# Performance work log

Hardware: AMD Instinct MI355X
Metric: run time of the kernel (lower is better)

## Reference

```python
import jax, jax.numpy as jnp
import numpy as np

B = 131072      # batch
UNITS = 32      # state dim (Dense output)
HID = 1024      # hard-coded hidden width in HopfieldLayer
DT = 0.1
T = 1.0
N_STEPS = int(round(T / DT))  # 10 RK4 steps


def setup_inputs() -> dict:
    key = jax.random.key(0)
    k0, k1, k2 = jax.random.split(key, 3)
    x = jax.random.normal(k0, (B, UNITS), dtype=jnp.float32)
    # glorot-uniform style init as in keras Dense defaults (scale only matters for realism)
    lim1 = float(np.sqrt(6.0 / (UNITS + HID)))
    lim2 = float(np.sqrt(6.0 / (HID + UNITS)))
    W1 = jax.random.uniform(k1, (UNITS, HID), jnp.float32, -lim1, lim1)
    W2 = jax.random.uniform(k2, (HID, UNITS), jnp.float32, -lim2, lim2)
    b1 = jnp.zeros((HID,), jnp.float32)
    b2 = jnp.zeros((UNITS,), jnp.float32)
    return {"x": x, "W1": W1, "b1": b1, "W2": W2, "b2": b2}


def reference(x, W1, b1, W2, b2):
    dt = jnp.float32(DT)

    def energy_sum(z):
        # E(z) = 8 * || Dense2(relu(Dense1(z))) ||_2  (per sample), summed over batch
        h = jax.nn.relu(z @ W1 + b1)          # [B, HID]
        y = h @ W2 + b2                        # [B, UNITS]
        return jnp.sum(8.0 * jnp.sqrt(jnp.sum(y * y, axis=1)))

    def pvf(z):
        # Hopfield phase vector field: dx/dt = -grad_x E(x); linear_transform = identity
        return -jax.grad(energy_sum)(z)

    def rk4_step(z, _):
        k1 = pvf(z)
        k2 = pvf(z + 0.5 * dt * k1)
        k3 = pvf(z + 0.5 * dt * k2)
        k4 = pvf(z + dt * k3)
        z_next = z + (dt / 6.0) * (k1 + 2.0 * k2 + 2.0 * k3 + k4)
        return z_next, None

    y, _ = jax.lax.scan(rk4_step, x, None, length=N_STEPS)
    return y
```

## Files before the change

### kernel.cpp

```cpp
#include <hip/hip_runtime.h>

typedef _Float16 f16;
typedef __attribute__((ext_vector_type(8))) _Float16 f16x8;
typedef __attribute__((ext_vector_type(16))) float f32x16;
typedef __attribute__((ext_vector_type(2))) unsigned int u32x2;
typedef __attribute__((ext_vector_type(4))) unsigned int u32x4;
typedef unsigned int u32;
typedef unsigned short u16;

#define UNITS 32
#define HID   1024
#define NCH   32
#define TPB   256
#define WPB   4
#define SPB   128
#define NBLK  1024
#define BWDOFF 262144

static_assert(NBLK * SPB == 131072, "grid covers batch");

__global__ void prep_weights(const float* __restrict__ W1,
                             const float* __restrict__ W2,
                             f16* __restrict__ ws) {
    int idx = blockIdx.x * 256 + threadIdx.x;
    int c = idx >> 10, rem = idx & 1023;
    int jl = rem >> 5, u = rem & 31;
    int j = c * 32 + jl;
    float w1 = W1[u * HID + j];
    f16 h1 = (f16)w1;
    f16 l1 = (f16)(w1 - (float)h1);
    float w2 = W2[j * UNITS + u];
    f16 h2 = (f16)w2;
    f16 l2 = (f16)(w2 - (float)h2);
    char* p = (char*)ws;
    auto off = [&](int region, int slice, int row, int k) {
        int ks = k >> 4;
        int lane = row + ((k >> 3) & 1) * 32;
        return region + c * 8192 + (slice * 2 + ks) * 1024 + lane * 16 + (k & 7) * 2;
    };
    *(f16*)(p + off(0, 0, jl, u))      = h1;
    *(f16*)(p + off(0, 1, jl, u))      = l1;
    *(f16*)(p + off(0, 2, u, jl))      = h2;
    *(f16*)(p + off(0, 3, u, jl))      = l2;
    *(f16*)(p + off(BWDOFF, 0, jl, u)) = h2;
    *(f16*)(p + off(BWDOFF, 1, jl, u)) = l2;
    *(f16*)(p + off(BWDOFF, 2, u, jl)) = h1;
    *(f16*)(p + off(BWDOFF, 3, u, jl)) = l1;
}

__device__ __forceinline__ void plswap(u32& a, u32& b) {
    u32x2 r = __builtin_amdgcn_permlane32_swap(a, b, false, false);
    a = r.x; b = r.y;
}

__device__ __forceinline__ float fmix_lo(u32 h, float v, float fone) {
    float r;
    asm("v_fma_mix_f32 %0, -%1, %2, %3 op_sel_hi:[1,0,0]"
        : "=v"(r) : "v"(h), "v"(fone), "v"(v));
    return r;
}
__device__ __forceinline__ float fmix_hi(u32 h, float v, float fone) {
    float r;
    asm("v_fma_mix_f32 %0, -%1, %2, %3 op_sel:[1,0,0] op_sel_hi:[1,0,0]"
        : "=v"(r) : "v"(h), "v"(fone), "v"(v));
    return r;
}

#define LOADSET4(S, base) {                                               \
    const char* p_ = (base);                                              \
    S##0 = *(const f16x8*)(p_);                                           \
    S##1 = *(const f16x8*)(p_ + 1024);                                    \
    S##2 = *(const f16x8*)(p_ + 2048);                                    \
    S##3 = *(const f16x8*)(p_ + 3072); }

#define BUILD_FRAGS(F0, F1, L0, L1, V) {                                  \
    u32 owh[8], owl[8];                                                   \
    _Pragma("unroll")                                                     \
    for (int i_ = 0; i_ < 8; ++i_) {                                      \
        float v0_ = (V)[2*i_], v1_ = (V)[2*i_ + 1];                       \
        auto hp_ = __builtin_amdgcn_cvt_pkrtz(v0_, v1_);                  \
        owh[i_] = __builtin_bit_cast(u32, hp_);                           \
        float r0_ = fmix_lo(owh[i_], v0_, fone);                          \
        float r1_ = fmix_hi(owh[i_], v1_, fone);                          \
        auto lp_ = __builtin_amdgcn_cvt_pkrtz(r0_, r1_);                  \
        owl[i_] = __builtin_bit_cast(u32, lp_);                           \
    }                                                                     \
    {                                                                     \
        u32 a0_ = owh[0], b0_ = owh[2]; plswap(a0_, b0_);                 \
        u32 a1_ = owh[1], b1_ = owh[3]; plswap(a1_, b1_);                 \
        F0 = __builtin_bit_cast(f16x8, (u32x4){a0_, a1_, b0_, b1_});      \
        u32 c0_ = owh[4], d0_ = owh[6]; plswap(c0_, d0_);                 \
        u32 c1_ = owh[5], d1_ = owh[7]; plswap(c1_, d1_);                 \
        F1 = __builtin_bit_cast(f16x8, (u32x4){c0_, c1_, d0_, d1_});      \
        u32 e0_ = owl[0], f0_ = owl[2]; plswap(e0_, f0_);                 \
        u32 e1_ = owl[1], f1_ = owl[3]; plswap(e1_, f1_);                 \
        L0 = __builtin_bit_cast(f16x8, (u32x4){e0_, e1_, f0_, f1_});      \
        u32 g0_ = owl[4], h0_ = owl[6]; plswap(g0_, h0_);                 \
        u32 g1_ = owl[5], h1_ = owl[7]; plswap(g1_, h1_);                 \
        L1 = __builtin_bit_cast(f16x8, (u32x4){g0_, g1_, h0_, h1_});      \
    } }

#define MFMA(d, a, b, c) d = __builtin_amdgcn_mfma_f32_32x32x16_f16(a, b, c, 0, 0, 0)

__global__ __launch_bounds__(TPB, 2)
__attribute__((amdgpu_waves_per_eu(2, 2)))
void hopfield_mfma4(const float* __restrict__ x,
                    const float* __restrict__ b1,
                    const float* __restrict__ b2,
                    const f16* __restrict__ ws,
                    float* __restrict__ out) {
    __shared__ __align__(16) float sB1p[HID];
    __shared__ __align__(16) float sB2p[UNITS];
    __shared__ u16 sMsk[WPB][NCH * 64];

    const int tid = threadIdx.x;
    const int wv = tid >> 6, ln = tid & 63;
    const int s32 = ln & 31, gh = ln >> 5;

    for (int i = tid; i < HID; i += TPB) {
        int c = i >> 5, g_ = (i >> 4) & 1, r = i & 15;
        sB1p[i] = b1[c * 32 + ((r & 3) + ((r >> 2) << 3) + (g_ << 2))];
    }
    if (tid < UNITS) {
        int g_ = (tid >> 4) & 1, r = tid & 15;
        sB2p[tid] = b2[(r & 3) + ((r >> 2) << 3) + (g_ << 2)];
    }
    __syncthreads();

    u16* mkb = &sMsk[wv][0];
    const float fone = 1.0f;

    const long samp = (long)blockIdx.x * SPB + wv * 32 + s32;
    float zb[16], acc[16];
    {
        const float* xr = x + samp * UNITS;
        #pragma unroll
        for (int q = 0; q < 4; ++q) {
            float4 v = *(const float4*)(xr + 8 * q + 4 * gh);
            zb[4*q+0] = v.x; zb[4*q+1] = v.y; zb[4*q+2] = v.z; zb[4*q+3] = v.w;
        }
    }

    f32x16 zeros;
    #pragma unroll
    for (int r = 0; r < 16; ++r) zeros[r] = 0.f;

    const char* pfwd = (const char*)ws + (size_t)ln * 16;
    const char* pbwd = pfwd + BWDOFF;

    f16x8 P0, P1, P2, P3;
    f16x8 Q0, Q1, Q2, Q3;
    LOADSET4(P, pfwd)

    f16x8 za0h, za1h, za0l, za1l;
    BUILD_FRAGS(za0h, za1h, za0l, za1l, zb)

    #pragma unroll 1
    for (int step = 0; step < 10; ++step) {
        #pragma unroll
        for (int r = 0; r < 16; ++r) acc[r] = 0.f;

        #pragma unroll 1
        for (int sub = 0; sub < 4; ++sub) {
            f32x16 ym;
            {
                const float4* bp = (const float4*)(sB2p + gh * 16);
                float4 v0 = bp[0], v1 = bp[1], v2 = bp[2], v3 = bp[3];
                ym[0]=v0.x; ym[1]=v0.y; ym[2]=v0.z; ym[3]=v0.w;
                ym[4]=v1.x; ym[5]=v1.y; ym[6]=v1.z; ym[7]=v1.w;
                ym[8]=v2.x; ym[9]=v2.y; ym[10]=v2.z; ym[11]=v2.w;
                ym[12]=v3.x; ym[13]=v3.y; ym[14]=v3.z; ym[15]=v3.w;
            }

            #pragma unroll 1
            for (int c = 0; c < NCH; ++c) {
                LOADSET4(Q, pfwd + c * 8192 + 4096)
                f32x16 hm;
                MFMA(hm, P0, za0h, zeros);
                MFMA(hm, P0, za0l, hm);
                MFMA(hm, P2, za0h, hm);
                MFMA(hm, P1, za1h, hm);
                MFMA(hm, P1, za1l, hm);
                MFMA(hm, P3, za1h, hm);

                float rv[16]; u32 mb = 0;
                {
                    const float4* bp = (const float4*)(sB1p + c * 32 + gh * 16);
                    float4 b0 = bp[0], b1v = bp[1], b2v = bp[2], b3 = bp[3];
                    float bv[16] = {b0.x,b0.y,b0.z,b0.w, b1v.x,b1v.y,b1v.z,b1v.w,
                                    b2v.x,b2v.y,b2v.z,b2v.w, b3.x,b3.y,b3.z,b3.w};
                    #pragma unroll
                    for (int r = 0; r < 16; ++r) {
                        float s = hm[r] + bv[r];
                        if (s > 0.f) mb |= (1u << r);
                        rv[r] = fmaxf(s, 0.f);
                    }
                }
                mkb[c * 64 + ln] = (u16)mb;

                f16x8 rf0, rf1, rl0, rl1;
                BUILD_FRAGS(rf0, rf1, rl0, rl1, rv)
                LOADSET4(P, (c < NCH - 1) ? (pfwd + (c + 1) * 8192) : pbwd)
                MFMA(ym, Q0, rf0, ym); MFMA(ym, Q0, rl0, ym);
                MFMA(ym, Q2, rf0, ym); MFMA(ym, Q1, rf1, ym);
                MFMA(ym, Q1, rl1, ym); MFMA(ym, Q3, rf1, ym);
            }

            f16x8 gf0, gf1, gl0, gl1;
            {
                float yv[16], t = 0.f;
                #pragma unroll
                for (int r = 0; r < 16; ++r) {
                    float y = ym[r];
                    yv[r] = y;
                    t = fmaf(y, y, t);
                }
                t += __shfl_xor(t, 32, 64);
                float s8 = 8.0f * rsqrtf(t);
                #pragma unroll
                for (int r = 0; r < 16; ++r) yv[r] *= s8;
                BUILD_FRAGS(gf0, gf1, gl0, gl1, yv)
            }

            f32x16 km;
            #pragma unroll
            for (int r = 0; r < 16; ++r) km[r] = 0.f;

            #pragma unroll 1
            for (int c = 0; c < NCH; ++c) {
                LOADSET4(Q, pbwd + c * 8192 + 4096)
                f32x16 gm;
                MFMA(gm, P0, gf0, zeros);
                MFMA(gm, P0, gl0, gm);
                MFMA(gm, P2, gf0, gm);
                MFMA(gm, P1, gf1, gm);
                MFMA(gm, P1, gl1, gm);
                MFMA(gm, P3, gf1, gm);

                u32 mb = mkb[c * 64 + ln];
                float mv[16];
                #pragma unroll
                for (int r = 0; r < 16; ++r) {
                    float g = gm[r];
                    mv[r] = (mb & (1u << r)) ? -g : 0.f;
                }

                f16x8 mf0, mf1, ml0, ml1;
                BUILD_FRAGS(mf0, mf1, ml0, ml1, mv)
                LOADSET4(P, (c < NCH - 1) ? (pbwd + (c + 1) * 8192) : pfwd)
                MFMA(km, Q0, mf0, km); MFMA(km, Q0, ml0, km);
                MFMA(km, Q2, mf0, km); MFMA(km, Q1, mf1, km);
                MFMA(km, Q1, ml1, km); MFMA(km, Q3, mf1, km);
            }

            if (sub < 3) {
                float aw = (sub == 0) ? 1.f : 2.f;
                float cw = (sub == 2) ? 0.1f : 0.05f;
                float vz[16];
                #pragma unroll
                for (int r = 0; r < 16; ++r) {
                    float kv = km[r];
                    acc[r] += aw * kv;
                    vz[r] = fmaf(cw, kv, zb[r]);
                }
                BUILD_FRAGS(za0h, za1h, za0l, za1l, vz)
            } else {
                #pragma unroll
                for (int r = 0; r < 16; ++r) acc[r] += km[r];
            }
        }

        #pragma unroll
        for (int r = 0; r < 16; ++r) zb[r] = fmaf(0.1f / 6.0f, acc[r], zb[r]);
        BUILD_FRAGS(za0h, za1h, za0l, za1l, zb)
    }

    {
        float* orow = out + samp * UNITS;
        #pragma unroll
        for (int q = 0; q < 4; ++q) {
            float4 v;
            v.x = zb[4*q+0]; v.y = zb[4*q+1]; v.z = zb[4*q+2]; v.w = zb[4*q+3];
            *(float4*)(orow + 8 * q + 4 * gh) = v;
        }
    }
}

extern "C" void kernel_launch(void* const* d_in, const int* in_sizes, int n_in,
                              void* d_out, int out_size, void* d_ws, size_t ws_size,
                              hipStream_t stream) {
    const float* x  = (const float*)d_in[0];
    const float* W1 = (const float*)d_in[1];
    const float* b1 = (const float*)d_in[2];
    const float* W2 = (const float*)d_in[3];
    const float* b2 = (const float*)d_in[4];
    float* out = (float*)d_out;
    f16* ws = (f16*)d_ws;
    hipLaunchKernelGGL(prep_weights, dim3(128), dim3(256), 0, stream, W1, W2, ws);
    hipLaunchKernelGGL(hopfield_mfma4, dim3(NBLK), dim3(TPB), 0, stream,
                       x, b1, b2, ws, out);
}
```

Baseline: 4.212 ms.

## Stage weight slices through double-buffered LDS via global_load_lds

Replaces per-wave direct global loads of each weight chunk with a cooperative block-wide async copy into a double-buffered LDS slice. Waves then read their MFMA operands from LDS. This is meant to cut redundant L2/global traffic, since all four waves previously fetched the same weights. The trade-off is a block barrier every chunk, which can stall waves, plus extra LDS reads and LDS footprint.

New measurement: 4.394 ms. 1.04x slower.

```diff
diff --git a/kernel.cpp b/kernel.cpp
--- a/kernel.cpp
+++ b/kernel.cpp
@@ -66,12 +66,20 @@
     return r;
 }
 
-#define LOADSET4(S, base) {                                               \
-    const char* p_ = (base);                                              \
-    S##0 = *(const f16x8*)(p_);                                           \
-    S##1 = *(const f16x8*)(p_ + 1024);                                    \
-    S##2 = *(const f16x8*)(p_ + 2048);                                    \
-    S##3 = *(const f16x8*)(p_ + 3072); }
+__device__ __forceinline__ void gload16(const void* g, void* l) {
+    __builtin_amdgcn_global_load_lds(
+        (const __attribute__((address_space(1))) void*)g,
+        (__attribute__((address_space(3))) void*)l, 16, 0, 0);
+}
+
+#define STAGE(bufw, gbase) {                                              \
+    const char* g_ = (gbase) + wv * 1024 + ln * 16;                       \
+    char* l_ = (char*)&sSlice[bufw][0] + wv * 1024;                       \
+    gload16(g_, l_);                                                      \
+    gload16(g_ + 4096, l_ + 4096); }
+
+#define LDB(dst, bufr, li)                                                \
+    dst = *(const f16x8*)((const char*)&sSlice[bufr][0] + (li) * 1024 + ln * 16);
 
 #define BUILD_FRAGS(F0, F1, L0, L1, V) {                                  \
     u32 owh[8], owl[8];                                                   \
@@ -104,11 +112,12 @@
 
 __global__ __launch_bounds__(TPB, 2)
 __attribute__((amdgpu_waves_per_eu(2, 2)))
-void hopfield_mfma4(const float* __restrict__ x,
+void hopfield_mfma5(const float* __restrict__ x,
                     const float* __restrict__ b1,
                     const float* __restrict__ b2,
                     const f16* __restrict__ ws,
                     float* __restrict__ out) {
+    __shared__ __align__(16) f16 sSlice[2][4096];
     __shared__ __align__(16) float sB1p[HID];
     __shared__ __align__(16) float sB2p[UNITS];
     __shared__ u16 sMsk[WPB][NCH * 64];
@@ -145,15 +154,13 @@
     #pragma unroll
     for (int r = 0; r < 16; ++r) zeros[r] = 0.f;
 
-    const char* pfwd = (const char*)ws + (size_t)ln * 16;
-    const char* pbwd = pfwd + BWDOFF;
-
-    f16x8 P0, P1, P2, P3;
-    f16x8 Q0, Q1, Q2, Q3;
-    LOADSET4(P, pfwd)
+    const char* pfwd_g = (const char*)ws;
+    const char* pbwd_g = pfwd_g + BWDOFF;
 
     f16x8 za0h, za1h, za0l, za1l;
     BUILD_FRAGS(za0h, za1h, za0l, za1l, zb)
+
+    STAGE(0, pfwd_g)
 
     #pragma unroll 1
     for (int step = 0; step < 10; ++step) {
@@ -174,14 +181,20 @@
 
             #pragma unroll 1
             for (int c = 0; c < NCH; ++c) {
-                LOADSET4(Q, pfwd + c * 8192 + 4096)
+                int buf = c & 1;
+                __syncthreads();
+                if (c < NCH - 1) { STAGE(buf ^ 1, pfwd_g + (c + 1) * 8192) }
+                else             { STAGE(buf ^ 1, pbwd_g) }
+
+                f16x8 w0, w1f, w2f, w3;
+                LDB(w0, buf, 0) LDB(w1f, buf, 1) LDB(w2f, buf, 2) LDB(w3, buf, 3)
                 f32x16 hm;
-                MFMA(hm, P0, za0h, zeros);
-                MFMA(hm, P0, za0l, hm);
-                MFMA(hm, P2, za0h, hm);
-                MFMA(hm, P1, za1h, hm);
-                MFMA(hm, P1, za1l, hm);
-                MFMA(hm, P3, za1h, hm);
+                MFMA(hm, w0, za0h, zeros);
+                MFMA(hm, w0, za0l, hm);
+                MFMA(hm, w2f, za0h, hm);
+                MFMA(hm, w1f, za1h, hm);
+                MFMA(hm, w1f, za1l, hm);
+                MFMA(hm, w3, za1h, hm);
 
                 float rv[16]; u32 mb = 0;
                 {
@@ -200,10 +213,10 @@
 
                 f16x8 rf0, rf1, rl0, rl1;
                 BUILD_FRAGS(rf0, rf1, rl0, rl1, rv)
-                LOADSET4(P, (c < NCH - 1) ? (pfwd + (c + 1) * 8192) : pbwd)
-                MFMA(ym, Q0, rf0, ym); MFMA(ym, Q0, rl0, ym);
-                MFMA(ym, Q2, rf0, ym); MFMA(ym, Q1, rf1, ym);
-                MFMA(ym, Q1, rl1, ym); MFMA(ym, Q3, rf1, ym);
+                LDB(w0, buf, 4) LDB(w1f, buf, 5) LDB(w2f, buf, 6) LDB(w3, buf, 7)
+                MFMA(ym, w0, rf0, ym); MFMA(ym, w0, rl0, ym);
+                MFMA(ym, w2f, rf0, ym); MFMA(ym, w1f, rf1, ym);
+                MFMA(ym, w1f, rl1, ym); MFMA(ym, w3, rf1, ym);
             }
 
             f16x8 gf0, gf1, gl0, gl1;
@@ -228,14 +241,20 @@
 
             #pragma unroll 1
             for (int c = 0; c < NCH; ++c) {
-                LOADSET4(Q, pbwd + c * 8192 + 4096)
+                int buf = c & 1;
+                __syncthreads();
+                if (c < NCH - 1) { STAGE(buf ^ 1, pbwd_g + (c + 1) * 8192) }
+                else             { STAGE(buf ^ 1, pfwd_g) }
+
+                f16x8 w0, w1f, w2f, w3;
+                LDB(w0, buf, 0) LDB(w1f, buf, 1) LDB(w2f, buf, 2) LDB(w3, buf, 3)
                 f32x16 gm;
-                MFMA(gm, P0, gf0, zeros);
-                MFMA(gm, P0, gl0, gm);
-                MFMA(gm, P2, gf0, gm);
-                MFMA(gm, P1, gf1, gm);
-                MFMA(gm, P1, gl1, gm);
-                MFMA(gm, P3, gf1, gm);
+                MFMA(gm, w0, gf0, zeros);
+                MFMA(gm, w0, gl0, gm);
+                MFMA(gm, w2f, gf0, gm);
+                MFMA(gm, w1f, gf1, gm);
+                MFMA(gm, w1f, gl1, gm);
+                MFMA(gm, w3, gf1, gm);
 
                 u32 mb = mkb[c * 64 + ln];
                 float mv[16];
@@ -247,10 +266,10 @@
 
                 f16x8 mf0, mf1, ml0, ml1;
                 BUILD_FRAGS(mf0, mf1, ml0, ml1, mv)
-                LOADSET4(P, (c < NCH - 1) ? (pbwd + (c + 1) * 8192) : pfwd)
-                MFMA(km, Q0, mf0, km); MFMA(km, Q0, ml0, km);
-                MFMA(km, Q2, mf0, km); MFMA(km, Q1, mf1, km);
-                MFMA(km, Q1, ml1, km); MFMA(km, Q3, mf1, km);
+                LDB(w0, buf, 4) LDB(w1f, buf, 5) LDB(w2f, buf, 6) LDB(w3, buf, 7)
+                MFMA(km, w0, mf0, km); MFMA(km, w0, ml0, km);
+                MFMA(km, w2f, mf0, km); MFMA(km, w1f, mf1, km);
+                MFMA(km, w1f, ml1, km); MFMA(km, w3, mf1, km);
             }
 
             if (sub < 3) {
@@ -297,6 +316,6 @@
     float* out = (float*)d_out;
     f16* ws = (f16*)d_ws;
     hipLaunchKernelGGL(prep_weights, dim3(128), dim3(256), 0, stream, W1, W2, ws);
-    hipLaunchKernelGGL(hopfield_mfma4, dim3(NBLK), dim3(TPB), 0, stream,
+    hipLaunchKernelGGL(hopfield_mfma5, dim3(NBLK), dim3(TPB), 0, stream,
                        x, b1, b2, ws, out);
 }
```

## Process two 32-sample tiles per wave to reuse loaded weight fragments

Applied to the files above, without the earlier changes.

Each wave now handles 64 samples as two independent 32-sample tiles, A and B. Every weight fragment loaded from global memory feeds two MFMA chains instead of one, and the grid shrinks to 512 blocks. This halves weight traffic per sample and interleaves independent MFMAs to hide latency. In exchange it raises register pressure (double accumulators and fragments) under the 2-waves-per-EU bound, doubles the mask shared memory, and leaves fewer blocks for 256 CUs (two per CU), which risks spills and lower occupancy.

Result: faster. 3.774 ms (-10.4%).

```diff
diff --git a/kernel.cpp b/kernel.cpp
--- a/kernel.cpp
+++ b/kernel.cpp
@@ -13,8 +13,8 @@
 #define NCH   32
 #define TPB   256
 #define WPB   4
-#define SPB   128
-#define NBLK  1024
+#define SPB   256
+#define NBLK  512
 #define BWDOFF 262144
 
 static_assert(NBLK * SPB == 131072, "grid covers batch");
@@ -102,16 +102,25 @@
 
 #define MFMA(d, a, b, c) d = __builtin_amdgcn_mfma_f32_32x32x16_f16(a, b, c, 0, 0, 0)
 
+#define RELU_MASK(RV, MB, HM, BV) {                                       \
+    MB = 0;                                                               \
+    _Pragma("unroll")                                                     \
+    for (int r_ = 0; r_ < 16; ++r_) {                                     \
+        float s_ = HM[r_] + BV[r_];                                       \
+        if (s_ > 0.f) MB |= (1u << r_);                                   \
+        RV[r_] = fmaxf(s_, 0.f);                                          \
+    } }
+
 __global__ __launch_bounds__(TPB, 2)
 __attribute__((amdgpu_waves_per_eu(2, 2)))
-void hopfield_mfma4(const float* __restrict__ x,
+void hopfield_mfma7(const float* __restrict__ x,
                     const float* __restrict__ b1,
                     const float* __restrict__ b2,
                     const f16* __restrict__ ws,
                     float* __restrict__ out) {
     __shared__ __align__(16) float sB1p[HID];
     __shared__ __align__(16) float sB2p[UNITS];
-    __shared__ u16 sMsk[WPB][NCH * 64];
+    __shared__ u16 sMsk[WPB][NCH * 128];
 
     const int tid = threadIdx.x;
     const int wv = tid >> 6, ln = tid & 63;
@@ -130,14 +139,17 @@
     u16* mkb = &sMsk[wv][0];
     const float fone = 1.0f;
 
-    const long samp = (long)blockIdx.x * SPB + wv * 32 + s32;
-    float zb[16], acc[16];
+    const long samp = (long)blockIdx.x * SPB + wv * 64 + s32;
+    float zbA[16], zbB[16], accA[16], accB[16];
     {
-        const float* xr = x + samp * UNITS;
+        const float* xa = x + samp * UNITS;
+        const float* xb = x + (samp + 32) * UNITS;
         #pragma unroll
         for (int q = 0; q < 4; ++q) {
-            float4 v = *(const float4*)(xr + 8 * q + 4 * gh);
-            zb[4*q+0] = v.x; zb[4*q+1] = v.y; zb[4*q+2] = v.z; zb[4*q+3] = v.w;
+            float4 va = *(const float4*)(xa + 8 * q + 4 * gh);
+            float4 vb = *(const float4*)(xb + 8 * q + 4 * gh);
+            zbA[4*q+0] = va.x; zbA[4*q+1] = va.y; zbA[4*q+2] = va.z; zbA[4*q+3] = va.w;
+            zbB[4*q+0] = vb.x; zbB[4*q+1] = vb.y; zbB[4*q+2] = vb.z; zbB[4*q+3] = vb.w;
         }
     }
 
@@ -152,136 +164,167 @@
     f16x8 Q0, Q1, Q2, Q3;
     LOADSET4(P, pfwd)
 
-    f16x8 za0h, za1h, za0l, za1l;
-    BUILD_FRAGS(za0h, za1h, za0l, za1l, zb)
+    f16x8 zaA0h, zaA1h, zaA0l, zaA1l;
+    f16x8 zaB0h, zaB1h, zaB0l, zaB1l;
+    BUILD_FRAGS(zaA0h, zaA1h, zaA0l, zaA1l, zbA)
+    BUILD_FRAGS(zaB0h, zaB1h, zaB0l, zaB1l, zbB)
 
     #pragma unroll 1
     for (int step = 0; step < 10; ++step) {
         #pragma unroll
-        for (int r = 0; r < 16; ++r) acc[r] = 0.f;
+        for (int r = 0; r < 16; ++r) { accA[r] = 0.f; accB[r] = 0.f; }
 
         #pragma unroll 1
         for (int sub = 0; sub < 4; ++sub) {
-            f32x16 ym;
+            f32x16 ymA, ymB;
             {
                 const float4* bp = (const float4*)(sB2p + gh * 16);
                 float4 v0 = bp[0], v1 = bp[1], v2 = bp[2], v3 = bp[3];
-                ym[0]=v0.x; ym[1]=v0.y; ym[2]=v0.z; ym[3]=v0.w;
-                ym[4]=v1.x; ym[5]=v1.y; ym[6]=v1.z; ym[7]=v1.w;
-                ym[8]=v2.x; ym[9]=v2.y; ym[10]=v2.z; ym[11]=v2.w;
-                ym[12]=v3.x; ym[13]=v3.y; ym[14]=v3.z; ym[15]=v3.w;
+                ymA[0]=v0.x; ymA[1]=v0.y; ymA[2]=v0.z; ymA[3]=v0.w;
+                ymA[4]=v1.x; ymA[5]=v1.y; ymA[6]=v1.z; ymA[7]=v1.w;
+                ymA[8]=v2.x; ymA[9]=v2.y; ymA[10]=v2.z; ymA[11]=v2.w;
+                ymA[12]=v3.x; ymA[13]=v3.y; ymA[14]=v3.z; ymA[15]=v3.w;
+                #pragma unroll
+                for (int r = 0; r < 16; ++r) ymB[r] = ymA[r];
             }
 
             #pragma unroll 1
             for (int c = 0; c < NCH; ++c) {
                 LOADSET4(Q, pfwd + c * 8192 + 4096)
-                f32x16 hm;
-                MFMA(hm, P0, za0h, zeros);
-                MFMA(hm, P0, za0l, hm);
-                MFMA(hm, P2, za0h, hm);
-                MFMA(hm, P1, za1h, hm);
-                MFMA(hm, P1, za1l, hm);
-                MFMA(hm, P3, za1h, hm);
-
-                float rv[16]; u32 mb = 0;
+                f32x16 hmA, hmB;
+                MFMA(hmA, P0, zaA0h, zeros); MFMA(hmB, P0, zaB0h, zeros);
+                MFMA(hmA, P0, zaA0l, hmA);   MFMA(hmB, P0, zaB0l, hmB);
+                MFMA(hmA, P2, zaA0h, hmA);   MFMA(hmB, P2, zaB0h, hmB);
+                MFMA(hmA, P1, zaA1h, hmA);   MFMA(hmB, P1, zaB1h, hmB);
+                MFMA(hmA, P1, zaA1l, hmA);   MFMA(hmB, P1, zaB1l, hmB);
+                MFMA(hmA, P3, zaA1h, hmA);   MFMA(hmB, P3, zaB1h, hmB);
+
+                float bv[16];
                 {
                     const float4* bp = (const float4*)(sB1p + c * 32 + gh * 16);
                     float4 b0 = bp[0], b1v = bp[1], b2v = bp[2], b3 = bp[3];
-                    float bv[16] = {b0.x,b0.y,b0.z,b0.w, b1v.x,b1v.y,b1v.z,b1v.w,
-                                    b2v.x,b2v.y,b2v.z,b2v.w, b3.x,b3.y,b3.z,b3.w};
-                    #pragma unroll
-                    for (int r = 0; r < 16; ++r) {
-                        float s = hm[r] + bv[r];
-                        if (s > 0.f) mb |= (1u << r);
-                        rv[r] = fmaxf(s, 0.f);
-                    }
-                }
-                mkb[c * 64 + ln] = (u16)mb;
-
-                f16x8 rf0, rf1, rl0, rl1;
-                BUILD_FRAGS(rf0, rf1, rl0, rl1, rv)
+                    bv[0]=b0.x; bv[1]=b0.y; bv[2]=b0.z; bv[3]=b0.w;
+                    bv[4]=b1v.x; bv[5]=b1v.y; bv[6]=b1v.z; bv[7]=b1v.w;
+                    bv[8]=b2v.x; bv[9]=b2v.y; bv[10]=b2v.z; bv[11]=b2v.w;
+                    bv[12]=b3.x; bv[13]=b3.y; bv[14]=b3.z; bv[15]=b3.w;
+                }
+                float rvA[16], rvB[16]; u32 mbA, mbB;
+                RELU_MASK(rvA, mbA, hmA, bv)
+                RELU_MASK(rvB, mbB, hmB, bv)
+                mkb[c * 128 + ln] = (u16)mbA;
+                mkb[c * 128 + 64 + ln] = (u16)mbB;
+
+                f16x8 rfA0, rfA1, rlA0, rlA1, rfB0, rfB1, rlB0, rlB1;
+                BUILD_FRAGS(rfA0, rfA1, rlA0, rlA1, rvA)
+                BUILD_FRAGS(rfB0, rfB1, rlB0, rlB1, rvB)
                 LOADSET4(P, (c < NCH - 1) ? (pfwd + (c + 1) * 8192) : pbwd)
-                MFMA(ym, Q0, rf0, ym); MFMA(ym, Q0, rl0, ym);
-                MFMA(ym, Q2, rf0, ym); MFMA(ym, Q1, rf1, ym);
-                MFMA(ym, Q1, rl1, ym); MFMA(ym, Q3, rf1, ym);
-            }
-
-            f16x8 gf0, gf1, gl0, gl1;
+                MFMA(ymA, Q0, rfA0, ymA); MFMA(ymB, Q0, rfB0, ymB);
+                MFMA(ymA, Q0, rlA0, ymA); MFMA(ymB, Q0, rlB0, ymB);
+                MFMA(ymA, Q2, rfA0, ymA); MFMA(ymB, Q2, rfB0, ymB);
+                MFMA(ymA, Q1, rfA1, ymA); MFMA(ymB, Q1, rfB1, ymB);
+                MFMA(ymA, Q1, rlA1, ymA); MFMA(ymB, Q1, rlB1, ymB);
+                MFMA(ymA, Q3, rfA1, ymA); MFMA(ymB, Q3, rfB1, ymB);
+            }
+
+            f16x8 gfA0, gfA1, glA0, glA1, gfB0, gfB1, glB0, glB1;
             {
                 float yv[16], t = 0.f;
                 #pragma unroll
                 for (int r = 0; r < 16; ++r) {
-                    float y = ym[r];
-                    yv[r] = y;
-                    t = fmaf(y, y, t);
+                    float y = ymA[r]; yv[r] = y; t = fmaf(y, y, t);
                 }
                 t += __shfl_xor(t, 32, 64);
                 float s8 = 8.0f * rsqrtf(t);
                 #pragma unroll
                 for (int r = 0; r < 16; ++r) yv[r] *= s8;
-                BUILD_FRAGS(gf0, gf1, gl0, gl1, yv)
-            }
-
-            f32x16 km;
+                BUILD_FRAGS(gfA0, gfA1, glA0, glA1, yv)
+            }
+            {
+                float yv[16], t = 0.f;
+                #pragma unroll
+                for (int r = 0; r < 16; ++r) {
+                    float y = ymB[r]; yv[r] = y; t = fmaf(y, y, t);
+                }
+                t += __shfl_xor(t, 32, 64);
+                float s8 = 8.0f * rsqrtf(t);
+                #pragma unroll
+                for (int r = 0; r < 16; ++r) yv[r] *= s8;
+                BUILD_FRAGS(gfB0, gfB1, glB0, glB1, yv)
+            }
+
+            f32x16 kmA, kmB;
             #pragma unroll
-            for (int r = 0; r < 16; ++r) km[r] = 0.f;
+            for (int r = 0; r < 16; ++r) { kmA[r] = 0.f; kmB[r] = 0.f; }
 
             #pragma unroll 1
             for (int c = 0; c < NCH; ++c) {
                 LOADSET4(Q, pbwd + c * 8192 + 4096)
-                f32x16 gm;
-                MFMA(gm, P0, gf0, zeros);
-                MFMA(gm, P0, gl0, gm);
-                MFMA(gm, P2, gf0, gm);
-                MFMA(gm, P1, gf1, gm);
-                MFMA(gm, P1, gl1, gm);
-                MFMA(gm, P3, gf1, gm);
-
-                u32 mb = mkb[c * 64 + ln];
-                float mv[16];
+                f32x16 gmA, gmB;
+                MFMA(gmA, P0, gfA0, zeros); MFMA(gmB, P0, gfB0, zeros);
+                MFMA(gmA, P0, glA0, gmA);   MFMA(gmB, P0, glB0, gmB);
+                MFMA(gmA, P2, gfA0, gmA);   MFMA(gmB, P2, gfB0, gmB);
+                MFMA(gmA, P1, gfA1, gmA);   MFMA(gmB, P1, gfB1, gmB);
+                MFMA(gmA, P1, glA1, gmA);   MFMA(gmB, P1, glB1, gmB);
+                MFMA(gmA, P3, gfA1, gmA);   MFMA(gmB, P3, gfB1, gmB);
+
+                u32 mbA = mkb[c * 128 + ln];
+                u32 mbB = mkb[c * 128 + 64 + ln];
+                float mvA[16], mvB[16];
                 #pragma unroll
                 for (int r = 0; r < 16; ++r) {
-                    float g = gm[r];
-                    mv[r] = (mb & (1u << r)) ? -g : 0.f;
-                }
-
-                f16x8 mf0, mf1, ml0, ml1;
-                BUILD_FRAGS(mf0, mf1, ml0, ml1, mv)
+                    mvA[r] = (mbA & (1u << r)) ? -gmA[r] : 0.f;
+                    mvB[r] = (mbB & (1u << r)) ? -gmB[r] : 0.f;
+                }
+
+                f16x8 mfA0, mfA1, mlA0, mlA1, mfB0, mfB1, mlB0, mlB1;
+                BUILD_FRAGS(mfA0, mfA1, mlA0, mlA1, mvA)
+                BUILD_FRAGS(mfB0, mfB1, mlB0, mlB1, mvB)
                 LOADSET4(P, (c < NCH - 1) ? (pbwd + (c + 1) * 8192) : pfwd)
-                MFMA(km, Q0, mf0, km); MFMA(km, Q0, ml0, km);
-                MFMA(km, Q2, mf0, km); MFMA(km, Q1, mf1, km);
-                MFMA(km, Q1, ml1, km); MFMA(km, Q3, mf1, km);
+                MFMA(kmA, Q0, mfA0, kmA); MFMA(kmB, Q0, mfB0, kmB);
+                MFMA(kmA, Q0, mlA0, kmA); MFMA(kmB, Q0, mlB0, kmB);
+                MFMA(kmA, Q2, mfA0, kmA); MFMA(kmB, Q2, mfB0, kmB);
+                MFMA(kmA, Q1, mfA1, kmA); MFMA(kmB, Q1, mfB1, kmB);
+                MFMA(kmA, Q1, mlA1, kmA); MFMA(kmB, Q1, mlB1, kmB);
+                MFMA(kmA, Q3, mfA1, kmA); MFMA(kmB, Q3, mfB1, kmB);
             }
 
             if (sub < 3) {
                 float aw = (sub == 0) ? 1.f : 2.f;
                 float cw = (sub == 2) ? 0.1f : 0.05f;
-                float vz[16];
+                float vzA[16], vzB[16];
                 #pragma unroll
                 for (int r = 0; r < 16; ++r) {
-                    float kv = km[r];
-                    acc[r] += aw * kv;
-                    vz[r] = fmaf(cw, kv, zb[r]);
-                }
-                BUILD_FRAGS(za0h, za1h, za0l, za1l, vz)
+                    float ka = kmA[r], kb = kmB[r];
+                    accA[r] += aw * ka;           accB[r] += aw * kb;
+                    vzA[r] = fmaf(cw, ka, zbA[r]); vzB[r] = fmaf(cw, kb, zbB[r]);
+                }
+                BUILD_FRAGS(zaA0h, zaA1h, zaA0l, zaA1l, vzA)
+                BUILD_FRAGS(zaB0h, zaB1h, zaB0l, zaB1l, vzB)
             } else {
                 #pragma unroll
-                for (int r = 0; r < 16; ++r) acc[r] += km[r];
+                for (int r = 0; r < 16; ++r) { accA[r] += kmA[r]; accB[r] += kmB[r]; }
             }
         }
 
         #pragma unroll
-        for (int r = 0; r < 16; ++r) zb[r] = fmaf(0.1f / 6.0f, acc[r], zb[r]);
-        BUILD_FRAGS(za0h, za1h, za0l, za1l, zb)
+        for (int r = 0; r < 16; ++r) {
+            zbA[r] = fmaf(0.1f / 6.0f, accA[r], zbA[r]);
+            zbB[r] = fmaf(0.1f / 6.0f, accB[r], zbB[r]);
+        }
+        BUILD_FRAGS(zaA0h, zaA1h, zaA0l, zaA1l, zbA)
+        BUILD_FRAGS(zaB0h, zaB1h, zaB0l, zaB1l, zbB)
     }
 
     {
-        float* orow = out + samp * UNITS;
+        float* oa = out + samp * UNITS;
+        float* ob = out + (samp + 32) * UNITS;
         #pragma unroll
         for (int q = 0; q < 4; ++q) {
-            float4 v;
-            v.x = zb[4*q+0]; v.y = zb[4*q+1]; v.z = zb[4*q+2]; v.w = zb[4*q+3];
-            *(float4*)(orow + 8 * q + 4 * gh) = v;
+            float4 va, vb;
+            va.x = zbA[4*q+0]; va.y = zbA[4*q+1]; va.z = zbA[4*q+2]; va.w = zbA[4*q+3];
+            vb.x = zbB[4*q+0]; vb.y = zbB[4*q+1]; vb.z = zbB[4*q+2]; vb.w = zbB[4*q+3];
+            *(float4*)(oa + 8 * q + 4 * gh) = va;
+            *(float4*)(ob + 8 * q + 4 * gh) = vb;
         }
     }
 }
@@ -297,6 +340,6 @@
     float* out = (float*)d_out;
     f16* ws = (f16*)d_ws;
     hipLaunchKernelGGL(prep_weights, dim3(128), dim3(256), 0, stream, W1, W2, ws);
-    hipLaunchKernelGGL(hopfield_mfma4, dim3(NBLK), dim3(TPB), 0, stream,
+    hipLaunchKernelGGL(hopfield_mfma7, dim3(NBLK), dim3(TPB), 0, stream,
                        x, b1, b2, ws, out);
 }
```
